# Kernel tuning notes

Measured on AMD Instinct MI355X. Metric: run time of the kernel, lower is better.

The kernel has to match this reference:

```python
import jax, jax.numpy as jnp
import numpy as np

B, LQ, LK = 4, 2048, 2048
DIM = 1024          # intermediate_dim
H, D = 16, 64       # num_heads, head_dim
AD = H * D          # attn_dim
SCALE = 1.0 / np.sqrt(D).astype(np.float32)


def setup_inputs() -> dict:
    key = jax.random.key(0)
    ks = jax.random.split(key, 12)
    init = lambda k, shape, fan_in: jax.random.normal(k, shape, jnp.float32) / np.sqrt(fan_in).astype(np.float32)
    return {
        "x": jax.random.normal(ks[0], (B, LQ, DIM), jnp.float32),
        "embeds": jax.random.normal(ks[1], (B, LK, DIM), jnp.float32),
        "Wq": init(ks[2], (DIM, AD), DIM), "bq": jnp.zeros((AD,), jnp.float32),
        "Wk": init(ks[3], (DIM, AD), DIM), "bk": jnp.zeros((AD,), jnp.float32),
        "Wv": init(ks[4], (DIM, AD), DIM), "bv": jnp.zeros((AD,), jnp.float32),
        "Wo": init(ks[5], (AD, DIM), AD), "bo": jnp.zeros((DIM,), jnp.float32),
    }


def reference(x, embeds, Wq, bq, Wk, bk, Wv, bv, Wo, bo):
    b, lq, _ = x.shape
    lk = embeds.shape[1]
    # separate QKV projections (cross-attention: K,V from embeds)
    q = (x @ Wq + bq).reshape(b, lq, H, D)
    k = (embeds @ Wk + bk).reshape(b, lk, H, D)
    v = (embeds @ Wv + bv).reshape(b, lk, H, D)
    # scaled dot-product attention; full [b,h,lq,lk] score matrix (as in source)
    scores = jnp.einsum("bqhd,bkhd->bhqk", q, k) * SCALE
    attn = jax.nn.softmax(scores, axis=-1)  # dropout is identity at eval
    ctx = jnp.einsum("bhqk,bkhd->bqhd", attn, v).reshape(b, lq, AD)
    return ctx @ Wo + bo
```

## Files before the change

### kernel.cpp

```cpp
#include <hip/hip_runtime.h>
#include <cstdint>
#include <cstddef>

#define NB   4
#define NLQ  2048
#define NLK  2048
#define NDIM 1024
#define NH   16
#define ND   64
#define NAD  1024

typedef __attribute__((ext_vector_type(8))) short bf16x8;
typedef __attribute__((ext_vector_type(4))) short sh4;
typedef __attribute__((ext_vector_type(4))) float f32x4;
typedef __attribute__((ext_vector_type(4))) int   i32x4;

static __device__ __forceinline__ short f2bf(float f) {
    unsigned u = __builtin_bit_cast(unsigned, f);
    u += 0x7fffu + ((u >> 16) & 1u);
    return (short)(u >> 16);
}

#define GLL16(GP, LP) __builtin_amdgcn_global_load_lds( \
    (const __attribute__((address_space(1))) void*)(GP), \
    (__attribute__((address_space(3))) void*)(LP), 16, 0, 0)

#define SYNC_LDS do { \
    __builtin_amdgcn_sched_barrier(0); \
    asm volatile("s_waitcnt lgkmcnt(0)" ::: "memory"); \
    __builtin_amdgcn_s_barrier(); \
    asm volatile("" ::: "memory"); \
    __builtin_amdgcn_sched_barrier(0); } while (0)

__global__ void cvt2(const float* __restrict__ x, const float* __restrict__ e,
                     short* __restrict__ xo, short* __restrict__ eo) {
    const float* in = blockIdx.y ? e : x;
    short* out = blockIdx.y ? eo : xo;
    int i = (blockIdx.x * blockDim.x + threadIdx.x) * 4;
    const float4 v = *(const float4*)(in + i);
    sh4 o;
    o.x = f2bf(v.x); o.y = f2bf(v.y); o.z = f2bf(v.z); o.w = f2bf(v.w);
    *(sh4*)(out + i) = o;
}

__global__ void wtrans4(const float* __restrict__ W0, const float* __restrict__ W1,
                        const float* __restrict__ W2, const float* __restrict__ W3,
                        short* __restrict__ T0, short* __restrict__ T1,
                        short* __restrict__ T2, short* __restrict__ T3) {
    __shared__ float t[32][33];
    const int z = blockIdx.z;
    const float* W = (z == 0) ? W0 : (z == 1) ? W1 : (z == 2) ? W2 : W3;
    short* Wt = (z == 0) ? T0 : (z == 1) ? T1 : (z == 2) ? T2 : T3;
    const int bx = blockIdx.x * 32;
    const int by = blockIdx.y * 32;
    const int tx = threadIdx.x & 31, ty = threadIdx.x >> 5;
    #pragma unroll
    for (int i = 0; i < 32; i += 8)
        t[ty + i][tx] = W[(size_t)(bx + ty + i) * 1024 + by + tx];
    __syncthreads();
    #pragma unroll
    for (int i = 0; i < 32; i += 8)
        Wt[(size_t)(by + ty + i) * 1024 + bx + tx] = f2bf(t[tx][ty + i]);
}


__global__ __launch_bounds__(256) void gemm_qkv(const short* __restrict__ Xb,
                                                const short* __restrict__ Eb,
                                                const short* __restrict__ Wqt,
                                                const short* __restrict__ Wkt,
                                                const short* __restrict__ Wvt,
                                                const float* __restrict__ bq,
                                                const float* __restrict__ bk,
                                                const float* __restrict__ bv,
                                                short* __restrict__ Qb,
                                                short* __restrict__ Kf,
                                                short* __restrict__ Vtb)
{
    const int N = 1024, K = 1024;
    __shared__ __align__(16) short As[128 * 64];
    __shared__ __align__(16) short Bs[128 * 64];
    const int z = blockIdx.z;
    const short* A    = (z == 0) ? Xb : Eb;
    const short* Wt   = (z == 0) ? Wqt : (z == 1) ? Wkt : Wvt;
    const float* bias = (z == 0) ? bq : (z == 1) ? bk : bv;
    const float scale = (z == 0) ? 0.18033688011112042f : 1.0f;

    const int tid = threadIdx.x, wave = tid >> 6, lane = tid & 63;
    const int quad = lane >> 4, col = lane & 15;
    const int m0 = blockIdx.x * 128, n0 = blockIdx.y * 128;
    const int wm = wave >> 1, wn = wave & 1;

    const f32x4 zero = {0.f, 0.f, 0.f, 0.f};
    f32x4 acc[4][4];
    #pragma unroll
    for (int i = 0; i < 4; ++i)
        #pragma unroll
        for (int j = 0; j < 4; ++j)
            acc[i][j] = zero;

    for (int kt = 0; kt < K / 64; ++kt) {
        __syncthreads();
        #pragma unroll
        for (int i = 0; i < 4; ++i) {
            const int f = (i * 4 + wave) * 512 + lane * 8;
            const int row = f >> 6, ch = (f >> 3) & 7;
            const int gcol = kt * 64 + ((ch ^ (row & 7)) * 8);
            GLL16(A  + (size_t)(m0 + row) * K + gcol, &As[f]);
            GLL16(Wt + (size_t)(n0 + row) * K + gcol, &Bs[f]);
        }
        __syncthreads();
        #pragma unroll
        for (int kk = 0; kk < 2; ++kk) {
            bf16x8 af[4], bfr[4];
            #pragma unroll
            for (int mt = 0; mt < 4; ++mt) {
                const int r = wm * 64 + mt * 16 + col;
                af[mt] = *(const bf16x8*)&As[r * 64 + (((kk * 4 + quad) ^ (r & 7)) * 8)];
            }
            #pragma unroll
            for (int nt = 0; nt < 4; ++nt) {
                const int r = wn * 64 + nt * 16 + col;
                bfr[nt] = *(const bf16x8*)&Bs[r * 64 + (((kk * 4 + quad) ^ (r & 7)) * 8)];
            }
            #pragma unroll
            for (int mt = 0; mt < 4; ++mt)
                #pragma unroll
                for (int nt = 0; nt < 4; ++nt)
                    acc[mt][nt] = __builtin_amdgcn_mfma_f32_16x16x32_bf16(af[mt], bfr[nt], acc[mt][nt], 0, 0, 0);
        }
    }

    if (z < 2) {
        short* outp = (z == 0) ? Qb : Kf;
        #pragma unroll
        for (int mt = 0; mt < 4; ++mt)
            #pragma unroll
            for (int nt = 0; nt < 4; ++nt) {
                const int n = n0 + wn * 64 + nt * 16 + col;
                const float bv_ = bias[n];
                #pragma unroll
                for (int r = 0; r < 4; ++r) {
                    const int m = m0 + wm * 64 + mt * 16 + quad * 4 + r;
                    outp[(size_t)m * N + n] = f2bf((acc[mt][nt][r] + bv_) * scale);
                }
            }
    } else {
        #pragma unroll
        for (int mt = 0; mt < 4; ++mt)
            #pragma unroll
            for (int nt = 0; nt < 4; ++nt) {
                const int n = n0 + wn * 64 + nt * 16 + col;
                const int hh = n >> 6, d = n & 63;
                const float bv_ = bias[n];
                const int mb = m0 + wm * 64 + mt * 16 + quad * 4;
                const int bb = mb >> 11, s = mb & 2047;
                sh4 o4;
                #pragma unroll
                for (int r = 0; r < 4; ++r)
                    o4[r] = f2bf(acc[mt][nt][r] + bv_);
                *(sh4*)&Vtb[((size_t)((bb * NH + hh) * 64 + d)) * NLK + s] = o4;
            }
    }
}

__global__ __launch_bounds__(256) void gemm_out(const short* __restrict__ A,
                                                const short* __restrict__ Wt,
                                                const float* __restrict__ bias,
                                                float* __restrict__ outp)
{
    const int N = 1024, K = 1024;
    __shared__ __align__(16) short As[128 * 64];
    __shared__ __align__(16) short Bs[128 * 64];
    const int tid = threadIdx.x, wave = tid >> 6, lane = tid & 63;
    const int quad = lane >> 4, col = lane & 15;
    const int m0 = blockIdx.x * 128, n0 = blockIdx.y * 128;
    const int wm = wave >> 1, wn = wave & 1;

    const f32x4 zero = {0.f, 0.f, 0.f, 0.f};
    f32x4 acc[4][4];
    #pragma unroll
    for (int i = 0; i < 4; ++i)
        #pragma unroll
        for (int j = 0; j < 4; ++j)
            acc[i][j] = zero;

    for (int kt = 0; kt < K / 64; ++kt) {
        __syncthreads();
        #pragma unroll
        for (int i = 0; i < 4; ++i) {
            const int f = (i * 4 + wave) * 512 + lane * 8;
            const int row = f >> 6, ch = (f >> 3) & 7;
            const int gcol = kt * 64 + ((ch ^ (row & 7)) * 8);
            GLL16(A  + (size_t)(m0 + row) * K + gcol, &As[f]);
            GLL16(Wt + (size_t)(n0 + row) * K + gcol, &Bs[f]);
        }
        __syncthreads();
        #pragma unroll
        for (int kk = 0; kk < 2; ++kk) {
            bf16x8 af[4], bfr[4];
            #pragma unroll
            for (int mt = 0; mt < 4; ++mt) {
                const int r = wm * 64 + mt * 16 + col;
                af[mt] = *(const bf16x8*)&As[r * 64 + (((kk * 4 + quad) ^ (r & 7)) * 8)];
            }
            #pragma unroll
            for (int nt = 0; nt < 4; ++nt) {
                const int r = wn * 64 + nt * 16 + col;
                bfr[nt] = *(const bf16x8*)&Bs[r * 64 + (((kk * 4 + quad) ^ (r & 7)) * 8)];
            }
            #pragma unroll
            for (int mt = 0; mt < 4; ++mt)
                #pragma unroll
                for (int nt = 0; nt < 4; ++nt)
                    acc[mt][nt] = __builtin_amdgcn_mfma_f32_16x16x32_bf16(af[mt], bfr[nt], acc[mt][nt], 0, 0, 0);
        }
    }

    #pragma unroll
    for (int mt = 0; mt < 4; ++mt)
        #pragma unroll
        for (int nt = 0; nt < 4; ++nt) {
            const int n = n0 + wn * 64 + nt * 16 + col;
            const float bv_ = bias[n];
            #pragma unroll
            for (int r = 0; r < 4; ++r) {
                const int m = m0 + wm * 64 + mt * 16 + quad * 4 + r;
                outp[(size_t)m * N + n] = acc[mt][nt][r] + bv_;
            }
        }
}

__global__ __launch_bounds__(512, 4) void attn_fused8(const short* __restrict__ Q,
                                                      const short* __restrict__ Kb,
                                                      const short* __restrict__ Vt,
                                                      short* __restrict__ ctx)
{
    __shared__ __align__(16) short Ks[2][64 * 64];
    __shared__ __align__(16) short Vs[2][64 * 64];
    const int tid = threadIdx.x, wave = tid >> 6, lane = tid & 63;
    const int quad = lane >> 4, col = lane & 15;

    const int p = blockIdx.x;
    const int g = ((p >> 3) & 7) * 8 + (p & 7);
    const int qt = p >> 6;
    const int h = g & 15, b = g >> 4;
    const int q0 = qt * 256 + wave * 32;

    bf16x8 aq[2][2];
    #pragma unroll
    for (int mt = 0; mt < 2; ++mt) {
        const short* qp = Q + (size_t)(b * NLQ + q0 + mt * 16 + col) * NAD + h * 64 + quad * 8;
        aq[mt][0] = *(const bf16x8*)qp;
        aq[mt][1] = *(const bf16x8*)(qp + 32);
    }

    bf16x8 vones;
    #pragma unroll
    for (int j = 0; j < 8; ++j) vones[j] = (short)0x3F80;

    const f32x4 zero = {0.f, 0.f, 0.f, 0.f};
    f32x4 O[4][2];
    f32x4 Ol[2];
    #pragma unroll
    for (int mt = 0; mt < 2; ++mt) {
        Ol[mt] = zero;
        #pragma unroll
        for (int db = 0; db < 4; ++db) O[db][mt] = zero;
    }

    const int srow = tid >> 3, schunk = tid & 7;
    const short* kbase = Kb + (size_t)b * NLK * NAD + h * 64 + schunk * 8;
    const short* vbase = Vt + (size_t)(b * NH + h) * 64 * NLK + schunk * 8;

    bf16x8 kv = *(const bf16x8*)(kbase + (size_t)srow * NAD);
    bf16x8 vv = *(const bf16x8*)(vbase + (size_t)srow * NLK);

    for (int kt = 0; kt < NLK / 64; ++kt) {
        short* Kw = &Ks[kt & 1][0];
        short* Vw = &Vs[kt & 1][0];
        {
            const int c = (schunk ^ (srow & 7)) * 8;
            *(bf16x8*)&Kw[srow * 64 + c] = kv;
            *(bf16x8*)&Vw[srow * 64 + c] = vv;
        }

        const int nk = (kt + 1) & (NLK / 64 - 1);
        kv = *(const bf16x8*)(kbase + (size_t)(nk * 64 + srow) * NAD);
        vv = *(const bf16x8*)(vbase + (size_t)srow * NLK + nk * 64);

        SYNC_LDS;

        bf16x8 kf[2][4];
        #pragma unroll
        for (int kk = 0; kk < 2; ++kk)
            #pragma unroll
            for (int nt = 0; nt < 4; ++nt) {
                const int key = nt * 16 + col;
                kf[kk][nt] = *(const bf16x8*)&Kw[key * 64 + (((kk * 4 + quad) ^ (key & 7)) * 8)];
            }

        int pk[2][2][4];
        #pragma unroll
        for (int mt = 0; mt < 2; ++mt) {
            f32x4 st[4];
            #pragma unroll
            for (int nt = 0; nt < 4; ++nt) st[nt] = zero;
            #pragma unroll
            for (int kk = 0; kk < 2; ++kk)
                #pragma unroll
                for (int nt = 0; nt < 4; ++nt)
                    st[nt] = __builtin_amdgcn_mfma_f32_16x16x32_bf16(kf[kk][nt], aq[mt][kk], st[nt], 0, 0, 0);
            #pragma unroll
            for (int nt = 0; nt < 4; ++nt) {
                const unsigned u0 = __builtin_bit_cast(unsigned, __builtin_amdgcn_exp2f(st[nt][0]));
                const unsigned u1 = __builtin_bit_cast(unsigned, __builtin_amdgcn_exp2f(st[nt][1]));
                const unsigned u2 = __builtin_bit_cast(unsigned, __builtin_amdgcn_exp2f(st[nt][2]));
                const unsigned u3 = __builtin_bit_cast(unsigned, __builtin_amdgcn_exp2f(st[nt][3]));
                const int t = nt >> 1, odd = (nt & 1) * 2;
                pk[mt][t][odd + 0] = (int)__builtin_amdgcn_perm(u1, u0, 0x07060302u);
                pk[mt][t][odd + 1] = (int)__builtin_amdgcn_perm(u3, u2, 0x07060302u);
            }
            #pragma unroll
            for (int t = 0; t < 2; ++t) {
                const bf16x8 pb = __builtin_bit_cast(bf16x8,
                    i32x4{pk[mt][t][0], pk[mt][t][1], pk[mt][t][2], pk[mt][t][3]});
                Ol[mt] = __builtin_amdgcn_mfma_f32_16x16x32_bf16(vones, pb, Ol[mt], 0, 0, 0);
            }
        }

        #pragma unroll
        for (int t = 0; t < 2; ++t)
            #pragma unroll
            for (int db = 0; db < 4; ++db) {
                const int row = db * 16 + col;
                const int c0 = t * 32 + quad * 4;
                const int c1 = t * 32 + 16 + quad * 4;
                const sh4 lo = *(const sh4*)&Vw[row * 64 + (((c0 >> 3) ^ (row & 7)) * 8 + (c0 & 7))];
                const sh4 hi = *(const sh4*)&Vw[row * 64 + (((c1 >> 3) ^ (row & 7)) * 8 + (c1 & 7))];
                bf16x8 va;
                #pragma unroll
                for (int j = 0; j < 4; ++j) { va[j] = lo[j]; va[j + 4] = hi[j]; }
                #pragma unroll
                for (int mt = 0; mt < 2; ++mt) {
                    const bf16x8 pb = __builtin_bit_cast(bf16x8,
                        i32x4{pk[mt][t][0], pk[mt][t][1], pk[mt][t][2], pk[mt][t][3]});
                    O[db][mt] = __builtin_amdgcn_mfma_f32_16x16x32_bf16(va, pb, O[db][mt], 0, 0, 0);
                }
            }
    }

    #pragma unroll
    for (int mt = 0; mt < 2; ++mt) {
        const float linv = 1.0f / Ol[mt][0];
        #pragma unroll
        for (int db = 0; db < 4; ++db) {
            sh4 o4;
            #pragma unroll
            for (int r = 0; r < 4; ++r)
                o4[r] = f2bf(O[db][mt][r] * linv);
            short* cp = ctx + (size_t)(b * NLQ + q0 + mt * 16 + col) * NAD
                      + h * 64 + db * 16 + quad * 4;
            *(sh4*)cp = o4;
        }
    }
}

extern "C" void kernel_launch(void* const* d_in, const int* in_sizes, int n_in,
                              void* d_out, int out_size, void* d_ws, size_t ws_size,
                              hipStream_t stream)
{
    (void)in_sizes; (void)n_in; (void)out_size; (void)ws_size;
    const float* x  = (const float*)d_in[0];
    const float* e  = (const float*)d_in[1];
    const float* Wq = (const float*)d_in[2];
    const float* bq = (const float*)d_in[3];
    const float* Wk = (const float*)d_in[4];
    const float* bk = (const float*)d_in[5];
    const float* Wv = (const float*)d_in[6];
    const float* bv = (const float*)d_in[7];
    const float* Wo = (const float*)d_in[8];
    const float* bo = (const float*)d_in[9];
    float* out = (float*)d_out;

    const size_t MQ = (size_t)NB * NLQ;
    short* wsp = (short*)d_ws;
    short* Xb  = wsp;
    short* Eb  = Xb  + MQ * NDIM;
    short* Wqt = Eb  + MQ * NDIM;
    short* Wkt = Wqt + (size_t)NDIM * NAD;
    short* Wvt = Wkt + (size_t)NDIM * NAD;
    short* Wot = Wvt + (size_t)NDIM * NAD;
    short* Qb  = Wot + (size_t)NDIM * NAD;
    short* Kf  = Qb  + MQ * NAD;
    short* Vtb = Kf  + MQ * NAD;
    short* Cx  = Vtb + MQ * NAD;

    cvt2<<<dim3(8192, 2), 256, 0, stream>>>(x, e, Xb, Eb);
    wtrans4<<<dim3(32, 32, 4), 256, 0, stream>>>(Wq, Wk, Wv, Wo, Wqt, Wkt, Wvt, Wot);

    gemm_qkv<<<dim3(64, 8, 3), 256, 0, stream>>>(Xb, Eb, Wqt, Wkt, Wvt,
                                                 bq, bk, bv, Qb, Kf, Vtb);

    attn_fused8<<<dim3(NB * NH * (NLQ / 256)), 512, 0, stream>>>(Qb, Kf, Vtb, Cx);

    gemm_out<<<dim3(64, 8), 256, 0, stream>>>(Cx, Wot, bo, out);
}
```

Baseline: 298.4 us.

## Remap GEMM tiles across XCDs, permute V smem layout, add MFMA priority hints

The QKV and output GEMMs now map linear block ids to tiles with an XCD-aware permutation, so neighbouring tiles that share operands land on the same chiplet's L2. In attention, V is stored into shared memory already permuted, so each PV operand becomes a single 16-byte LDS read instead of two 8-byte reads plus a repack; the stores become two 8-byte writes. s_setprio hints raise wave priority around MFMA bursts to improve interleaving with the exp/pack work.

```diff
diff --git a/kernel.cpp b/kernel.cpp
--- a/kernel.cpp
+++ b/kernel.cpp
@@ -61,6 +61,11 @@
     #pragma unroll
     for (int i = 0; i < 32; i += 8)
         Wt[(size_t)(by + ty + i) * 1024 + bx + tx] = f2bf(t[tx][ty + i]);
+}
+
+static __device__ __forceinline__ void xcd_tile_remap(int f, int& bx, int& by) {
+    bx = ((f & 7) << 3) | ((f >> 3) & 7);
+    by = f >> 6;
 }
 
 
@@ -87,7 +92,9 @@
 
     const int tid = threadIdx.x, wave = tid >> 6, lane = tid & 63;
     const int quad = lane >> 4, col = lane & 15;
-    const int m0 = blockIdx.x * 128, n0 = blockIdx.y * 128;
+    int bx, by;
+    xcd_tile_remap(blockIdx.x + (blockIdx.y << 6), bx, by);
+    const int m0 = bx * 128, n0 = by * 128;
     const int wm = wave >> 1, wn = wave & 1;
 
     const f32x4 zero = {0.f, 0.f, 0.f, 0.f};
@@ -173,7 +180,9 @@
     __shared__ __align__(16) short Bs[128 * 64];
     const int tid = threadIdx.x, wave = tid >> 6, lane = tid & 63;
     const int quad = lane >> 4, col = lane & 15;
-    const int m0 = blockIdx.x * 128, n0 = blockIdx.y * 128;
+    int bx, by;
+    xcd_tile_remap(blockIdx.x + (blockIdx.y << 6), bx, by);
+    const int m0 = bx * 128, n0 = by * 128;
     const int wm = wave >> 1, wn = wave & 1;
 
     const f32x4 zero = {0.f, 0.f, 0.f, 0.f};
@@ -230,10 +239,10 @@
         }
 }
 
-__global__ __launch_bounds__(512, 4) void attn_fused8(const short* __restrict__ Q,
-                                                      const short* __restrict__ Kb,
-                                                      const short* __restrict__ Vt,
-                                                      short* __restrict__ ctx)
+__global__ __launch_bounds__(512, 4) void attn_fused13(const short* __restrict__ Q,
+                                                       const short* __restrict__ Kb,
+                                                       const short* __restrict__ Vt,
+                                                       short* __restrict__ ctx)
 {
     __shared__ __align__(16) short Ks[2][64 * 64];
     __shared__ __align__(16) short Vs[2][64 * 64];
@@ -271,6 +280,10 @@
     const int srow = tid >> 3, schunk = tid & 7;
     const short* kbase = Kb + (size_t)b * NLK * NAD + h * 64 + schunk * 8;
     const short* vbase = Vt + (size_t)(b * NH + h) * 64 * NLK + schunk * 8;
+
+    const int vt_ = schunk >> 2, vh_ = (schunk >> 1) & 1, vq0 = (schunk * 2) & 3;
+    const int vcl = vt_ * 4 + vq0;
+    const int voff = vh_ * 4;
 
     bf16x8 kv = *(const bf16x8*)(kbase + (size_t)srow * NAD);
     bf16x8 vv = *(const bf16x8*)(vbase + (size_t)srow * NLK);
@@ -281,7 +294,10 @@
         {
             const int c = (schunk ^ (srow & 7)) * 8;
             *(bf16x8*)&Kw[srow * 64 + c] = kv;
-            *(bf16x8*)&Vw[srow * 64 + c] = vv;
+            const sh4 lo = { vv[0], vv[1], vv[2], vv[3] };
+            const sh4 hi = { vv[4], vv[5], vv[6], vv[7] };
+            *(sh4*)&Vw[srow * 64 + ((vcl ^ (srow & 7)) * 8 + voff)] = lo;
+            *(sh4*)&Vw[srow * 64 + (((vcl + 1) ^ (srow & 7)) * 8 + voff)] = hi;
         }
 
         const int nk = (kt + 1) & (NLK / 64 - 1);
@@ -305,11 +321,13 @@
             f32x4 st[4];
             #pragma unroll
             for (int nt = 0; nt < 4; ++nt) st[nt] = zero;
+            __builtin_amdgcn_s_setprio(1);
             #pragma unroll
             for (int kk = 0; kk < 2; ++kk)
                 #pragma unroll
                 for (int nt = 0; nt < 4; ++nt)
                     st[nt] = __builtin_amdgcn_mfma_f32_16x16x32_bf16(kf[kk][nt], aq[mt][kk], st[nt], 0, 0, 0);
+            __builtin_amdgcn_s_setprio(0);
             #pragma unroll
             for (int nt = 0; nt < 4; ++nt) {
                 const unsigned u0 = __builtin_bit_cast(unsigned, __builtin_amdgcn_exp2f(st[nt][0]));
@@ -320,12 +338,14 @@
                 pk[mt][t][odd + 0] = (int)__builtin_amdgcn_perm(u1, u0, 0x07060302u);
                 pk[mt][t][odd + 1] = (int)__builtin_amdgcn_perm(u3, u2, 0x07060302u);
             }
+            __builtin_amdgcn_s_setprio(1);
             #pragma unroll
             for (int t = 0; t < 2; ++t) {
                 const bf16x8 pb = __builtin_bit_cast(bf16x8,
                     i32x4{pk[mt][t][0], pk[mt][t][1], pk[mt][t][2], pk[mt][t][3]});
                 Ol[mt] = __builtin_amdgcn_mfma_f32_16x16x32_bf16(vones, pb, Ol[mt], 0, 0, 0);
             }
+            __builtin_amdgcn_s_setprio(0);
         }
 
         #pragma unroll
@@ -333,19 +353,15 @@
             #pragma unroll
             for (int db = 0; db < 4; ++db) {
                 const int row = db * 16 + col;
-                const int c0 = t * 32 + quad * 4;
-                const int c1 = t * 32 + 16 + quad * 4;
-                const sh4 lo = *(const sh4*)&Vw[row * 64 + (((c0 >> 3) ^ (row & 7)) * 8 + (c0 & 7))];
-                const sh4 hi = *(const sh4*)&Vw[row * 64 + (((c1 >> 3) ^ (row & 7)) * 8 + (c1 & 7))];
-                bf16x8 va;
-                #pragma unroll
-                for (int j = 0; j < 4; ++j) { va[j] = lo[j]; va[j + 4] = hi[j]; }
+                const bf16x8 va = *(const bf16x8*)&Vw[row * 64 + (((t * 4 + quad) ^ (row & 7)) * 8)];
+                __builtin_amdgcn_s_setprio(1);
                 #pragma unroll
                 for (int mt = 0; mt < 2; ++mt) {
                     const bf16x8 pb = __builtin_bit_cast(bf16x8,
                         i32x4{pk[mt][t][0], pk[mt][t][1], pk[mt][t][2], pk[mt][t][3]});
                     O[db][mt] = __builtin_amdgcn_mfma_f32_16x16x32_bf16(va, pb, O[db][mt], 0, 0, 0);
                 }
+                __builtin_amdgcn_s_setprio(0);
             }
     }
 
@@ -401,7 +417,7 @@
     gemm_qkv<<<dim3(64, 8, 3), 256, 0, stream>>>(Xb, Eb, Wqt, Wkt, Wvt,
                                                  bq, bk, bv, Qb, Kf, Vtb);
 
-    attn_fused8<<<dim3(NB * NH * (NLQ / 256)), 512, 0, stream>>>(Qb, Kf, Vtb, Cx);
+    attn_fused13<<<dim3(NB * NH * (NLQ / 256)), 512, 0, stream>>>(Qb, Kf, Vtb, Cx);
 
     gemm_out<<<dim3(64, 8), 256, 0, stream>>>(Cx, Wot, bo, out);
 }
```

Result: no change. 300.8 us (+0.8%).
